# Optimization experiments

Measured on AMD Instinct MI355X. Metric: run time of the kernel, lower is better.

The kernel has to match this reference:

```python
import jax, jax.numpy as jnp
import numpy as np

B, N, F, H, E, A = 16, 5000, 64, 32, 160000, 16


def setup_inputs() -> dict:
    key = jax.random.key(0)
    ks = jax.random.split(key, 11)
    features = jax.random.normal(ks[0], (B, N, F), jnp.float32)
    edge_index = jax.random.randint(ks[1], (2, E), 0, N, dtype=jnp.int64)
    # GCN layer params (glorot-ish scale)
    W1 = jax.random.normal(ks[2], (F, H), jnp.float32) / np.sqrt(F)
    b1 = jnp.zeros((H,), jnp.float32)
    W2 = jax.random.normal(ks[3], (H, H), jnp.float32) / np.sqrt(H)
    b2 = jnp.zeros((H,), jnp.float32)
    # policy MLP: Linear(N*H, 512) -> ReLU -> Linear(512, A)
    Wp1 = jax.random.normal(ks[4], (N * H, 512), jnp.float32) / np.sqrt(N * H)
    bp1 = jnp.zeros((512,), jnp.float32)
    Wp2 = jax.random.normal(ks[5], (512, A), jnp.float32) / np.sqrt(512)
    bp2 = jnp.zeros((A,), jnp.float32)
    return dict(features=features, edge_index=edge_index, W1=W1, b1=b1,
                W2=W2, b2=b2, Wp1=Wp1, bp1=bp1, Wp2=Wp2, bp2=bp2)


def gcn_layer(x, W, b, src, dst, n):
    # PyG GCNConv: D^{-1/2} (A + I) D^{-1/2} X W + b  (self-loops already in src/dst)
    deg = jnp.zeros((n,), x.dtype).at[dst].add(1.0)            # in-degree incl. self-loop
    dinv = jnp.where(deg > 0, jax.lax.rsqrt(deg), 0.0)
    norm = dinv[src] * dinv[dst]                               # [E+N]
    xw = jnp.einsum('bnf,fh->bnh', x, W)                       # transform first (F->H shrinks traffic)
    msg = xw[:, src, :] * norm[None, :, None]                  # gather + scale  [B, E+N, H]
    out = jnp.zeros((x.shape[0], n, W.shape[1]), x.dtype).at[:, dst, :].add(msg)  # scatter-add
    return out + b


def reference(features, edge_index, W1, b1, W2, b2, Wp1, bp1, Wp2, bp2):
    n = features.shape[1]
    loops = jnp.arange(n, dtype=edge_index.dtype)
    src = jnp.concatenate([edge_index[0], loops])
    dst = jnp.concatenate([edge_index[1], loops])
    h = jax.nn.relu(gcn_layer(features, W1, b1, src, dst, n))
    h = jax.nn.relu(gcn_layer(h, W2, b2, src, dst, n))
    flat = h.reshape(h.shape[0], -1)                           # [B, N*H]
    hid = jax.nn.relu(flat @ Wp1 + bp1)
    return hid @ Wp2 + bp2                                     # [B, n_actions]
```

## Files before the change

kernel.cpp:

```cpp
#include <hip/hip_runtime.h>
#include <hip/hip_bf16.h>

#define NB 16
#define NN 5000
#define NF 64
#define NH 32
#define NE 160000
#define NP 512
#define NA 16
#define KCH 250
#define KLEN 640


__global__ __launch_bounds__(256) void k_hist(const int* __restrict__ ei,
                                              int* __restrict__ deg) {
    int e = blockIdx.x * 256 + threadIdx.x;
    if (e < NE) atomicAdd(&deg[ei[NE + e]], 1);
}

__global__ __launch_bounds__(1024) void k_scan(const int* __restrict__ deg,
                                               int* __restrict__ offs,
                                               int* __restrict__ cursor,
                                               float* __restrict__ dinv) {
    __shared__ int sm[1024];
    int t = threadIdx.x;
    int v[5]; int sum = 0;
    int base = t * 5;
#pragma unroll
    for (int i = 0; i < 5; ++i) {
        int idx = base + i;
        int d = (idx < NN) ? deg[idx] : 0;
        v[i] = d; sum += d;
    }
    sm[t] = sum; __syncthreads();
    for (int off = 1; off < 1024; off <<= 1) {
        int x = (t >= off) ? sm[t - off] : 0;
        __syncthreads();
        sm[t] += x;
        __syncthreads();
    }
    int excl = (t == 0) ? 0 : sm[t - 1];
#pragma unroll
    for (int i = 0; i < 5; ++i) {
        int idx = base + i;
        if (idx < NN) {
            offs[idx] = excl; cursor[idx] = excl;
            dinv[idx] = 1.0f / sqrtf((float)(v[i] + 1));
            excl += v[i];
        }
    }
    if (t == 1023) offs[NN] = sm[1023];
}

__global__ __launch_bounds__(256) void k_fill(const int* __restrict__ ei,
                                              const float* __restrict__ dinv,
                                              int* __restrict__ cursor,
                                              int2* __restrict__ pack) {
    int e = blockIdx.x * 256 + threadIdx.x;
    if (e < NE) {
        int s = ei[e];
        int d = ei[NE + e];
        float nrm = dinv[s] * dinv[d];
        int pos = atomicAdd(&cursor[d], 1);
        pack[pos] = make_int2(s, __float_as_int(nrm));
    }
}


__global__ __launch_bounds__(256) void k_xform1(const float* __restrict__ feat,
                                                const float* __restrict__ W1,
                                                float* __restrict__ xw) {
    __shared__ float w1s[NF * NH];
    int t = threadIdx.x;
    for (int i = t; i < NF * NH; i += 256) w1s[i] = W1[i];
    __syncthreads();
    int h = t & 31;
    int rg = t >> 5;
    int r0 = blockIdx.x * 32 + rg * 4;
    const float4* f4 = (const float4*)feat;
    float acc0 = 0.f, acc1 = 0.f, acc2 = 0.f, acc3 = 0.f;
#pragma unroll
    for (int q = 0; q < 16; ++q) {
        float4 a0 = f4[(size_t)(r0 + 0) * 16 + q];
        float4 a1 = f4[(size_t)(r0 + 1) * 16 + q];
        float4 a2 = f4[(size_t)(r0 + 2) * 16 + q];
        float4 a3 = f4[(size_t)(r0 + 3) * 16 + q];
        float w0 = w1s[(q * 4 + 0) * NH + h];
        float w1_ = w1s[(q * 4 + 1) * NH + h];
        float w2_ = w1s[(q * 4 + 2) * NH + h];
        float w3_ = w1s[(q * 4 + 3) * NH + h];
        acc0 += a0.x * w0; acc0 += a0.y * w1_; acc0 += a0.z * w2_; acc0 += a0.w * w3_;
        acc1 += a1.x * w0; acc1 += a1.y * w1_; acc1 += a1.z * w2_; acc1 += a1.w * w3_;
        acc2 += a2.x * w0; acc2 += a2.y * w1_; acc2 += a2.z * w2_; acc2 += a2.w * w3_;
        acc3 += a3.x * w0; acc3 += a3.y * w1_; acc3 += a3.z * w2_; acc3 += a3.w * w3_;
    }
    xw[(size_t)(r0 + 0) * NH + h] = acc0;
    xw[(size_t)(r0 + 1) * NH + h] = acc1;
    xw[(size_t)(r0 + 2) * NH + h] = acc2;
    xw[(size_t)(r0 + 3) * NH + h] = acc3;
}


__device__ __forceinline__ void agg_decode(int bid, int tid, int& b, int& n,
                                           int& hp, int& half) {
    int xcd = bid & 7;
    int g = bid >> 3;
    int hi = (g >= 1250) ? 1 : 0;
    b = xcd * 2 + hi;
    int ng = g - hi * 1250;
    int w = tid >> 6;
    n = ng * 4 + w;
    int lane = tid & 63;
    hp = lane & 31;
    half = lane >> 5;
}

__global__ __launch_bounds__(256) void k_agg1(const float* __restrict__ xw,
                                              const int* __restrict__ offs,
                                              const float* __restrict__ dinv,
                                              const int2* __restrict__ pack,
                                              const float* __restrict__ b1,
                                              float* __restrict__ out) {
    int b, n, hp, half;
    agg_decode(blockIdx.x, threadIdx.x, b, n, hp, half);
    const float* inb = xw + (size_t)b * (NN * NH);
    int s0 = offs[n], s1 = offs[n + 1];
    float acc = 0.f;
    for (int e = s0 + half; e < s1; e += 2) {
        int2 p = pack[e];
        acc += __int_as_float(p.y) * inb[(size_t)p.x * NH + hp];
    }
    acc += __shfl_xor(acc, 32);
    float di = dinv[n];
    float v = acc + di * di * inb[(size_t)n * NH + hp] + b1[hp];
    v = fmaxf(v, 0.f);
    if ((threadIdx.x & 63) < 32)
        out[(size_t)b * (NN * NH) + (size_t)n * NH + hp] = v;
}


__global__ __launch_bounds__(256) void k_agg2(const float* __restrict__ h1,
                                              const int* __restrict__ offs,
                                              const float* __restrict__ dinv,
                                              const int2* __restrict__ pack,
                                              const float* __restrict__ W2,
                                              const float* __restrict__ b2,
                                              float* __restrict__ h2) {
    int b, n, hp, half;
    agg_decode(blockIdx.x, threadIdx.x, b, n, hp, half);
    float w2c[NH];
#pragma unroll
    for (int kh = 0; kh < NH; ++kh) w2c[kh] = W2[kh * NH + hp];
    const float* inb = h1 + (size_t)b * (NN * NH);
    int s0 = offs[n], s1 = offs[n + 1];
    float acc = 0.f;
    for (int e = s0 + half; e < s1; e += 2) {
        int2 p = pack[e];
        acc += __int_as_float(p.y) * inb[(size_t)p.x * NH + hp];
    }
    acc += __shfl_xor(acc, 32);
    float di = dinv[n];
    float aggv = acc + di * di * inb[(size_t)n * NH + hp];
    float o = b2[hp];
#pragma unroll
    for (int kh = 0; kh < NH; ++kh) {
        float av = __uint_as_float(__builtin_amdgcn_readlane(__float_as_uint(aggv), kh));
        o += av * w2c[kh];
    }
    o = fmaxf(o, 0.f);
    if ((threadIdx.x & 63) < 32)
        h2[(size_t)b * (NN * NH) + (size_t)n * NH + hp] = o;
}


__global__ __launch_bounds__(512) void k_gemm1(const float* __restrict__ flat,
                                               const float* __restrict__ Wp1,
                                               float* __restrict__ part) {
    __shared__ __align__(16) float sT[64 * 20];
    int t = threadIdx.x;
    int c4 = t & 127;
    int mq = t >> 7;
    int lane = t & 63;
    int r2 = t >> 6;
    int k0 = blockIdx.x * KLEN;
    float acc[4][4] = {{0.f}};
    for (int sub = 0; sub < KLEN / 64; ++sub) {
        int kb = k0 + sub * 64;
#pragma unroll
        for (int i = 0; i < 2; ++i) {
            int m = r2 * 2 + i;
            sT[lane * 20 + m] = flat[(size_t)m * (NN * NH) + kb + lane];
        }
        __syncthreads();
#pragma unroll 4
        for (int kk = 0; kk < 64; ++kk) {
            float4 w = *(const float4*)(Wp1 + (size_t)(kb + kk) * NP + c4 * 4);
            float4 f = *(const float4*)(sT + kk * 20 + mq * 4);
            acc[0][0] += f.x * w.x; acc[0][1] += f.x * w.y; acc[0][2] += f.x * w.z; acc[0][3] += f.x * w.w;
            acc[1][0] += f.y * w.x; acc[1][1] += f.y * w.y; acc[1][2] += f.y * w.z; acc[1][3] += f.y * w.w;
            acc[2][0] += f.z * w.x; acc[2][1] += f.z * w.y; acc[2][2] += f.z * w.z; acc[2][3] += f.z * w.w;
            acc[3][0] += f.w * w.x; acc[3][1] += f.w * w.y; acc[3][2] += f.w * w.z; acc[3][3] += f.w * w.w;
        }
        __syncthreads();
    }
    float* p = part + (size_t)blockIdx.x * (NB * NP);
#pragma unroll
    for (int i = 0; i < 4; ++i) {
        float4 o = make_float4(acc[i][0], acc[i][1], acc[i][2], acc[i][3]);
        *(float4*)(p + (mq * 4 + i) * NP + c4 * 4) = o;
    }
}

__global__ __launch_bounds__(256) void k_reduce(const float* __restrict__ part,
                                                const float* __restrict__ bp1,
                                                float* __restrict__ hid) {
    int o = blockIdx.x * 256 + threadIdx.x;
    float s = bp1[o & (NP - 1)];
#pragma unroll 10
    for (int ch = 0; ch < KCH; ++ch) s += part[(size_t)ch * (NB * NP) + o];
    hid[o] = fmaxf(s, 0.f);
}


__global__ __launch_bounds__(256) void k_gemm2(const float* __restrict__ hid,
                                               const float* __restrict__ Wp2,
                                               const float* __restrict__ bp2,
                                               float* __restrict__ out) {
    int t = threadIdx.x;
    int m = t >> 4, a = t & 15;
    int ks = blockIdx.x * 64;
    float acc = (blockIdx.x == 0) ? bp2[a] : 0.f;
#pragma unroll
    for (int k = 0; k < 64; k += 4) {
        float4 hv = *(const float4*)(hid + m * NP + ks + k);
        acc += hv.x * Wp2[(ks + k + 0) * NA + a];
        acc += hv.y * Wp2[(ks + k + 1) * NA + a];
        acc += hv.z * Wp2[(ks + k + 2) * NA + a];
        acc += hv.w * Wp2[(ks + k + 3) * NA + a];
    }
    atomicAdd(out + m * NA + a, acc);
}


static inline size_t align256(size_t x) { return (x + 255) & ~(size_t)255; }

extern "C" void kernel_launch(void* const* d_in, const int* in_sizes, int n_in,
                              void* d_out, int out_size, void* d_ws, size_t ws_size,
                              hipStream_t stream) {
    const float* feat = (const float*)d_in[0];
    const int*   ei   = (const int*)d_in[1];
    const float* W1   = (const float*)d_in[2];
    const float* b1   = (const float*)d_in[3];
    const float* W2   = (const float*)d_in[4];
    const float* b2   = (const float*)d_in[5];
    const float* Wp1  = (const float*)d_in[6];
    const float* bp1  = (const float*)d_in[7];
    const float* Wp2  = (const float*)d_in[8];
    const float* bp2  = (const float*)d_in[9];
    float* out = (float*)d_out;

    char* w = (char*)d_ws;
    size_t off = 0;
    int*   deg    = (int*)(w + off);   off = align256(off + NN * 4);
    int*   offs   = (int*)(w + off);   off = align256(off + (NN + 1) * 4);
    int*   cursor = (int*)(w + off);   off = align256(off + NN * 4);
    float* dinv   = (float*)(w + off); off = align256(off + NN * 4);
    int2*  pack   = (int2*)(w + off);  off = align256(off + (size_t)NE * 8);
    float* bufA   = (float*)(w + off); off = align256(off + (size_t)NB * NN * NH * 4);
    float* bufB   = (float*)(w + off); off = align256(off + (size_t)NB * NN * NH * 4);
    float* hid    = (float*)(w + off); off = align256(off + (size_t)NB * NP * 4);
    (void)ws_size; (void)n_in; (void)in_sizes; (void)out_size;

    hipMemsetAsync(deg, 0, NN * 4, stream);
    hipMemsetAsync(out, 0, NB * NA * 4, stream);

    k_hist<<<(NE + 255) / 256, 256, 0, stream>>>(ei, deg);
    k_scan<<<1, 1024, 0, stream>>>(deg, offs, cursor, dinv);
    k_fill<<<(NE + 255) / 256, 256, 0, stream>>>(ei, dinv, cursor, pack);

    k_xform1<<<(NB * NN) / 32, 256, 0, stream>>>(feat, W1, bufA);
    k_agg1<<<NB * (NN / 4), 256, 0, stream>>>(bufA, offs, dinv, pack, b1, bufB);
    k_agg2<<<NB * (NN / 4), 256, 0, stream>>>(bufB, offs, dinv, pack, W2, b2, bufA);

    k_gemm1<<<KCH, 512, 0, stream>>>(bufA, Wp1, bufB);
    k_reduce<<<(NB * NP) / 256, 256, 0, stream>>>(bufB, bp1, hid);
    k_gemm2<<<NP / 64, 256, 0, stream>>>(hid, Wp2, bp2, out);
}
```

Measured before the change: 713.6 us.

## Double split-K chunks, prefetch edge packs, and split reduction with atomics

Halves the K length per gemm1 block so twice as many blocks cover the large Wp1 stream, adds a launch-bounds occupancy hint and deeper unroll, and stores partials in a dedicated buffer. The reduction is split across four y-blocks with atomic accumulation into a zeroed hid, and the bias+ReLU moves into gemm2. Edge aggregation software-prefetches the next packed edge before the gather to hide index-load latency. The extra partials double the partial-sum traffic, and the atomics make summation order nondeterministic.

```diff
diff --git a/kernel.cpp b/kernel.cpp
--- a/kernel.cpp
+++ b/kernel.cpp
@@ -8,8 +8,8 @@
 #define NE 160000
 #define NP 512
 #define NA 16
-#define KCH 250
-#define KLEN 640
+#define KCH 500
+#define KLEN 320
 
 
 __global__ __launch_bounds__(256) void k_hist(const int* __restrict__ ei,
@@ -115,6 +115,24 @@
     half = lane >> 5;
 }
 
+__device__ __forceinline__ float edge_agg(const int2* __restrict__ pack,
+                                          const float* __restrict__ inb,
+                                          int s0, int s1, int half, int hp) {
+    float acc = 0.f;
+    int e = s0 + half;
+    bool have = e < s1;
+    int2 p = have ? pack[e] : make_int2(0, 0);
+    while (have) {
+        int2 cur = p;
+        int en = e + 2;
+        bool hn = en < s1;
+        if (hn) p = pack[en];
+        acc += __int_as_float(cur.y) * inb[(size_t)cur.x * NH + hp];
+        e = en; have = hn;
+    }
+    return acc;
+}
+
 __global__ __launch_bounds__(256) void k_agg1(const float* __restrict__ xw,
                                               const int* __restrict__ offs,
                                               const float* __restrict__ dinv,
@@ -125,11 +143,7 @@
     agg_decode(blockIdx.x, threadIdx.x, b, n, hp, half);
     const float* inb = xw + (size_t)b * (NN * NH);
     int s0 = offs[n], s1 = offs[n + 1];
-    float acc = 0.f;
-    for (int e = s0 + half; e < s1; e += 2) {
-        int2 p = pack[e];
-        acc += __int_as_float(p.y) * inb[(size_t)p.x * NH + hp];
-    }
+    float acc = edge_agg(pack, inb, s0, s1, half, hp);
     acc += __shfl_xor(acc, 32);
     float di = dinv[n];
     float v = acc + di * di * inb[(size_t)n * NH + hp] + b1[hp];
@@ -153,11 +167,7 @@
     for (int kh = 0; kh < NH; ++kh) w2c[kh] = W2[kh * NH + hp];
     const float* inb = h1 + (size_t)b * (NN * NH);
     int s0 = offs[n], s1 = offs[n + 1];
-    float acc = 0.f;
-    for (int e = s0 + half; e < s1; e += 2) {
-        int2 p = pack[e];
-        acc += __int_as_float(p.y) * inb[(size_t)p.x * NH + hp];
-    }
+    float acc = edge_agg(pack, inb, s0, s1, half, hp);
     acc += __shfl_xor(acc, 32);
     float di = dinv[n];
     float aggv = acc + di * di * inb[(size_t)n * NH + hp];
@@ -173,9 +183,9 @@
 }
 
 
-__global__ __launch_bounds__(512) void k_gemm1(const float* __restrict__ flat,
-                                               const float* __restrict__ Wp1,
-                                               float* __restrict__ part) {
+__global__ __launch_bounds__(512, 4) void k_gemm1(const float* __restrict__ flat,
+                                                  const float* __restrict__ Wp1,
+                                                  float* __restrict__ part) {
     __shared__ __align__(16) float sT[64 * 20];
     int t = threadIdx.x;
     int c4 = t & 127;
@@ -192,7 +202,7 @@
             sT[lane * 20 + m] = flat[(size_t)m * (NN * NH) + kb + lane];
         }
         __syncthreads();
-#pragma unroll 4
+#pragma unroll 8
         for (int kk = 0; kk < 64; ++kk) {
             float4 w = *(const float4*)(Wp1 + (size_t)(kb + kk) * NP + c4 * 4);
             float4 f = *(const float4*)(sT + kk * 20 + mq * 4);
@@ -212,17 +222,18 @@
 }
 
 __global__ __launch_bounds__(256) void k_reduce(const float* __restrict__ part,
-                                                const float* __restrict__ bp1,
                                                 float* __restrict__ hid) {
     int o = blockIdx.x * 256 + threadIdx.x;
-    float s = bp1[o & (NP - 1)];
-#pragma unroll 10
-    for (int ch = 0; ch < KCH; ++ch) s += part[(size_t)ch * (NB * NP) + o];
-    hid[o] = fmaxf(s, 0.f);
+    int c0 = blockIdx.y * (KCH / 4);
+    float s = 0.f;
+#pragma unroll 5
+    for (int ch = c0; ch < c0 + KCH / 4; ++ch) s += part[(size_t)ch * (NB * NP) + o];
+    atomicAdd(&hid[o], s);
 }
 
 
 __global__ __launch_bounds__(256) void k_gemm2(const float* __restrict__ hid,
+                                               const float* __restrict__ bp1,
                                                const float* __restrict__ Wp2,
                                                const float* __restrict__ bp2,
                                                float* __restrict__ out) {
@@ -233,10 +244,15 @@
 #pragma unroll
     for (int k = 0; k < 64; k += 4) {
         float4 hv = *(const float4*)(hid + m * NP + ks + k);
-        acc += hv.x * Wp2[(ks + k + 0) * NA + a];
-        acc += hv.y * Wp2[(ks + k + 1) * NA + a];
-        acc += hv.z * Wp2[(ks + k + 2) * NA + a];
-        acc += hv.w * Wp2[(ks + k + 3) * NA + a];
+        float4 bv = *(const float4*)(bp1 + ks + k);
+        float h0 = fmaxf(hv.x + bv.x, 0.f);
+        float h1 = fmaxf(hv.y + bv.y, 0.f);
+        float h2 = fmaxf(hv.z + bv.z, 0.f);
+        float h3 = fmaxf(hv.w + bv.w, 0.f);
+        acc += h0 * Wp2[(ks + k + 0) * NA + a];
+        acc += h1 * Wp2[(ks + k + 1) * NA + a];
+        acc += h2 * Wp2[(ks + k + 2) * NA + a];
+        acc += h3 * Wp2[(ks + k + 3) * NA + a];
     }
     atomicAdd(out + m * NA + a, acc);
 }
@@ -268,10 +284,12 @@
     int2*  pack   = (int2*)(w + off);  off = align256(off + (size_t)NE * 8);
     float* bufA   = (float*)(w + off); off = align256(off + (size_t)NB * NN * NH * 4);
     float* bufB   = (float*)(w + off); off = align256(off + (size_t)NB * NN * NH * 4);
+    float* part   = (float*)(w + off); off = align256(off + (size_t)KCH * NB * NP * 4);
     float* hid    = (float*)(w + off); off = align256(off + (size_t)NB * NP * 4);
     (void)ws_size; (void)n_in; (void)in_sizes; (void)out_size;
 
     hipMemsetAsync(deg, 0, NN * 4, stream);
+    hipMemsetAsync(hid, 0, NB * NP * 4, stream);
     hipMemsetAsync(out, 0, NB * NA * 4, stream);
 
     k_hist<<<(NE + 255) / 256, 256, 0, stream>>>(ei, deg);
@@ -282,7 +300,7 @@
     k_agg1<<<NB * (NN / 4), 256, 0, stream>>>(bufA, offs, dinv, pack, b1, bufB);
     k_agg2<<<NB * (NN / 4), 256, 0, stream>>>(bufB, offs, dinv, pack, W2, b2, bufA);
 
-    k_gemm1<<<KCH, 512, 0, stream>>>(bufA, Wp1, bufB);
-    k_reduce<<<(NB * NP) / 256, 256, 0, stream>>>(bufB, bp1, hid);
-    k_gemm2<<<NP / 64, 256, 0, stream>>>(hid, Wp2, bp2, out);
-}
+    k_gemm1<<<KCH, 512, 0, stream>>>(bufA, Wp1, part);
+    k_reduce<<<dim3(NB * NP / 256, 4), 256, 0, stream>>>(part, hid);
+    k_gemm2<<<NP / 64, 256, 0, stream>>>(hid, bp1, Wp2, bp2, out);
+}
```

After: 673.2 us. 1.06x faster.
